# Optimization experiments

Measured on AMD Instinct MI355X. Metric: run time of the kernel, lower is better.

Reference implementation:

```python
import jax, jax.numpy as jnp
import numpy as np

N_FFT = 4096
HOP = 1024
HALF = N_FFT // 2  # 2048; also number of freq bins is HALF+1 = 2049


def _make_kernels():
    # Periodic hann window, matching torch.hann_window(N) default (periodic=True)
    n = np.arange(N_FFT, dtype=np.float32)
    window = 0.5 * (1.0 - np.cos(2.0 * np.pi * n / N_FFT))
    freqs = np.arange(HALF + 1, dtype=np.float32)[:, None]  # [K,1]
    omega = 2.0 * np.pi * freqs * n[None, :] / N_FFT        # [K, n_fft]
    scale = np.float32(1.0 / np.sqrt(N_FFT))                # normalized=True
    cos_k = (np.cos(omega) * window[None, :] * scale).astype(np.float32)
    sin_k = (-np.sin(omega) * window[None, :] * scale).astype(np.float32)
    return jnp.asarray(cos_k), jnp.asarray(sin_k)


def setup_inputs() -> dict:
    key = jax.random.key(0)
    x = jax.random.normal(key, (32, 1, 441000), dtype=jnp.float32)
    cos_kernel, sin_kernel = _make_kernels()  # each [2049, 4096]
    return {"x": x, "cos_kernel": cos_kernel, "sin_kernel": sin_kernel}


def reference(x, cos_kernel, sin_kernel):
    # center=True: reflect-pad half_n_fft on each side of the time axis
    xp = jnp.pad(x, ((0, 0), (0, 0), (HALF, HALF)), mode='reflect')  # [B,1,L]
    L = xp.shape[-1]
    num_frames = (L - N_FFT) // HOP + 1
    # Frame extraction (equivalent to stride-HOP conv1d with width-N_FFT kernels)
    idx = HOP * jnp.arange(num_frames)[:, None] + jnp.arange(N_FFT)[None, :]  # [F, n_fft]
    frames = xp[:, 0, :][:, idx]  # [B, F, n_fft]
    real = jnp.einsum('bfn,kn->bkf', frames, cos_kernel)  # [B, 2049, F]
    imag = jnp.einsum('bfn,kn->bkf', frames, sin_kernel)  # [B, 2049, F]
    return jnp.stack((real, imag), axis=-1)  # [B, 2049, F, 2]
```

## Files before the change

kernel.cpp:

```cpp
#include <hip/hip_runtime.h>
#include <math.h>

#define NFFT  4096
#define MHALF 2048
#define HOPSZ 1024
#define LX    441000
#define NB    32
#define NF    431
#define NK    2049
#define NFPB  8
#define FBLK  54
#define NWG3  (NB * FBLK)
#define CH3   (NWG3 / 8)

#define SW(A) ((A) ^ (((A) >> 4) & 0xF))
#define SOFTSYNC() asm volatile("" ::: "memory")

typedef __fp16 half2v __attribute__((ext_vector_type(2)));

__device__ __forceinline__ float2 cadd(float2 a, float2 b){ return make_float2(a.x+b.x, a.y+b.y); }
__device__ __forceinline__ float2 csub(float2 a, float2 b){ return make_float2(a.x-b.x, a.y-b.y); }
__device__ __forceinline__ float2 cmul(float2 a, float2 b){
  return make_float2(fmaf(a.x, b.x, -(a.y*b.y)), fmaf(a.x, b.y, a.y*b.x));
}
#define STH(ptr, idx, v) (ptr)[idx] = __builtin_amdgcn_cvt_pkrtz((v).x, (v).y)
__device__ __forceinline__ float2 ldh(const half2v* __restrict__ X, int idx) {
  half2v h = X[idx];
  return make_float2((float)h.x, (float)h.y);
}

constexpr float W32C[22] = {
  1.0f, 0.98078528040323f, 0.92387953251129f, 0.83146961230255f, 0.70710678118655f,
  0.55557023301960f, 0.38268343236509f, 0.19509032201613f, 0.0f, -0.19509032201613f,
  -0.38268343236509f, -0.55557023301960f, -0.70710678118655f, -0.83146961230255f,
  -0.92387953251129f, -0.98078528040323f, -1.0f, -0.98078528040323f,
  -0.92387953251129f, -0.83146961230255f, -0.70710678118655f, -0.55557023301960f };
constexpr float W32S[22] = {
  0.0f, 0.19509032201613f, 0.38268343236509f, 0.55557023301960f, 0.70710678118655f,
  0.83146961230255f, 0.92387953251129f, 0.98078528040323f, 1.0f, 0.98078528040323f,
  0.92387953251129f, 0.83146961230255f, 0.70710678118655f, 0.55557023301960f,
  0.38268343236509f, 0.19509032201613f, 0.0f, -0.19509032201613f,
  -0.38268343236509f, -0.55557023301960f, -0.70710678118655f, -0.83146961230255f };

template<int N> __device__ __forceinline__ float2 w32m(float2 z) {
  if constexpr (N == 0) { return z; }
  else if constexpr (N == 8) { return make_float2(z.y, -z.x); }
  else {
    constexpr float c = W32C[N];
    constexpr float s = W32S[N];
    return make_float2(fmaf(z.x, c, z.y * s), fmaf(z.y, c, -(z.x * s)));
  }
}

__global__ void stft_init(float* __restrict__ ws) {
  int i = blockIdx.x * blockDim.x + threadIdx.x;
  const double PI = 3.14159265358979323846;
  if (i < 4096) {
    double w = 0.5 * (1.0 - cos(2.0 * PI * (double)i / 4096.0)) * (1.0 / 64.0);
    ws[i] = (float)w;
  }
  if (i < 1024) {
    double a = -2.0 * PI * (double)i / 2048.0;
    ws[4096 + 2 * i]     = (float)cos(a);
    ws[4096 + 2 * i + 1] = (float)sin(a);
  }
  if (i < 2049) {
    double a = -2.0 * PI * (double)i / 4096.0;
    ws[6144 + 2 * i]     = (float)cos(a);
    ws[6144 + 2 * i + 1] = (float)sin(a);
  }
}

__device__ __forceinline__ void dft8(const float2* a, float2* B) {
  float2 t0 = cadd(a[0], a[4]), t1 = csub(a[0], a[4]);
  float2 t2 = cadd(a[2], a[6]), t3 = csub(a[2], a[6]);
  float2 t4 = cadd(a[1], a[5]), t5 = csub(a[1], a[5]);
  float2 t6 = cadd(a[3], a[7]), t7 = csub(a[3], a[7]);
  const float K = 0.70710678118654752f;
  float2 wt5  = make_float2(K * (t5.x + t5.y), K * (t5.y - t5.x));
  float2 w3t7 = make_float2(K * (t7.y - t7.x), -K * (t7.x + t7.y));
  float2 wt7  = make_float2(K * (t7.x + t7.y), K * (t7.y - t7.x));
  float2 w3t5 = make_float2(K * (t5.y - t5.x), -K * (t5.x + t5.y));
  float2 e0 = cadd(t0, t2), e1 = csub(t0, t2);
  float2 f0 = cadd(t4, t6), f1 = csub(t4, t6);
  B[0] = cadd(e0, f0);
  B[4] = csub(e0, f0);
  B[2] = make_float2(e1.x + f1.y, e1.y - f1.x);
  B[6] = make_float2(e1.x - f1.y, e1.y + f1.x);
  float2 g0 = make_float2(t1.x + t3.y, t1.y - t3.x);
  float2 g1 = make_float2(t1.x - t3.y, t1.y + t3.x);
  float2 h0 = cadd(wt5, w3t7);
  float2 h1 = cadd(wt7, w3t5);
  B[1] = cadd(g0, h0);
  B[5] = csub(g0, h0);
  B[3] = cadd(g1, h1);
  B[7] = csub(g1, h1);
}

template<int S>
__device__ __forceinline__ void bf8(half2v* __restrict__ X, int sxor,
                                    const float2* __restrict__ twg,
                                    int j, const float2* a) {
  const int q = j & (S - 1);
  const int t = j - q;
  float2 B[8];
  dft8(a, B);
  float2 w1 = twg[t];
  float2 w2 = cmul(w1, w1);
  float2 w3 = cmul(w2, w1);
  float2 w4 = cmul(w2, w2);
  float2 w5 = cmul(w3, w2);
  float2 w6 = cmul(w3, w3);
  float2 w7 = cmul(w4, w3);
  const int o = q + 8 * t;
  STH(X, SW(o) ^ sxor, B[0]);
  { float2 v = cmul(w1, B[1]); STH(X, SW(o + S)     ^ sxor, v); }
  { float2 v = cmul(w2, B[2]); STH(X, SW(o + 2 * S) ^ sxor, v); }
  { float2 v = cmul(w3, B[3]); STH(X, SW(o + 3 * S) ^ sxor, v); }
  { float2 v = cmul(w4, B[4]); STH(X, SW(o + 4 * S) ^ sxor, v); }
  { float2 v = cmul(w5, B[5]); STH(X, SW(o + 5 * S) ^ sxor, v); }
  { float2 v = cmul(w6, B[6]); STH(X, SW(o + 6 * S) ^ sxor, v); }
  { float2 v = cmul(w7, B[7]); STH(X, SW(o + 7 * S) ^ sxor, v); }
}

__device__ __forceinline__ void loadwin(float2 (*a)[8], const float* __restrict__ xb,
                                        int f, int l,
                                        const float2* __restrict__ winv,
                                        const float* __restrict__ win) {
  const int base = f * HOPSZ - MHALF;
  if (base >= 0 && base + NFFT <= LX) {
    const float2* xv = (const float2*)(xb + base);
#pragma unroll
    for (int r = 0; r < 4; ++r) {
      const int j = l + (r << 6);
#pragma unroll
      for (int m = 0; m < 8; ++m) {
        const int idx = j + (m << 8);
        float2 v = xv[idx];
        float2 w = winv[idx];
        a[r][m] = make_float2(v.x * w.x, v.y * w.y);
      }
    }
  } else {
#pragma unroll
    for (int r = 0; r < 4; ++r) {
      const int j = l + (r << 6);
#pragma unroll
      for (int m = 0; m < 8; ++m) {
        const int idx = j + (m << 8);
        int s0 = base + 2 * idx;
        int s1 = s0 + 1;
        s0 = (s0 < 0) ? -s0 : ((s0 >= LX) ? (2 * LX - 2 - s0) : s0);
        s1 = (s1 < 0) ? -s1 : ((s1 >= LX) ? (2 * LX - 2 - s1) : s1);
        a[r][m] = make_float2(xb[s0] * win[2 * idx], xb[s1] * win[2 * idx + 1]);
      }
    }
  }
}

#define VBLK(dd, slp, sx, V) do {                                     \
    float2 tt[8], BB[8];                                              \
    tt[0] = dd[8*(V)+0];                                              \
    tt[1] = w32m<1*(V)>(dd[8*(V)+1]);                                 \
    tt[2] = w32m<2*(V)>(dd[8*(V)+2]);                                 \
    tt[3] = w32m<3*(V)>(dd[8*(V)+3]);                                 \
    tt[4] = w32m<4*(V)>(dd[8*(V)+4]);                                 \
    tt[5] = w32m<5*(V)>(dd[8*(V)+5]);                                 \
    tt[6] = w32m<6*(V)>(dd[8*(V)+6]);                                 \
    tt[7] = w32m<7*(V)>(dd[8*(V)+7]);                                 \
    dft8(tt, BB);                                                     \
    STH(slp, SW(l + (((V) +  0) << 6)) ^ sx, BB[0]);                  \
    STH(slp, SW(l + (((V) +  4) << 6)) ^ sx, BB[1]);                  \
    STH(slp, SW(l + (((V) +  8) << 6)) ^ sx, BB[2]);                  \
    STH(slp, SW(l + (((V) + 12) << 6)) ^ sx, BB[3]);                  \
    STH(slp, SW(l + (((V) + 16) << 6)) ^ sx, BB[4]);                  \
    STH(slp, SW(l + (((V) + 20) << 6)) ^ sx, BB[5]);                  \
    STH(slp, SW(l + (((V) + 24) << 6)) ^ sx, BB[6]);                  \
    STH(slp, SW(l + (((V) + 28) << 6)) ^ sx, BB[7]);                  \
  } while (0)

#define DFT4PASS(dd) do {                                             \
    _Pragma("unroll")                                                 \
    for (int m1 = 0; m1 < 8; ++m1) {                                  \
      float2 p0 = dd[m1], p1 = dd[m1 + 8], p2 = dd[m1 + 16], p3 = dd[m1 + 24]; \
      float2 e0 = cadd(p0, p2), e1 = csub(p0, p2);                    \
      float2 o0 = cadd(p1, p3), o1 = csub(p1, p3);                    \
      dd[m1]      = cadd(e0, o0);                                     \
      dd[m1 + 8]  = make_float2(e1.x + o1.y, e1.y - o1.x);            \
      dd[m1 + 16] = csub(e0, o0);                                     \
      dd[m1 + 24] = make_float2(e1.x - o1.y, e1.y + o1.x);            \
    }                                                                 \
  } while (0)

__global__ __launch_bounds__(256, 2) void stft_fft(const float* __restrict__ x,
                                                   const float* __restrict__ ws,
                                                   float* __restrict__ out) {
  __shared__ half2v fbuf[NFPB * 2048];

  const int tid = threadIdx.x;
  const int wid = (blockIdx.x & 7) * CH3 + (blockIdx.x >> 3);
  const int b  = wid / FBLK;
  const int fb = wid - b * FBLK;
  const int f0 = fb * NFPB;
  const int wv = tid >> 6;
  const int l  = tid & 63;
  const int fA = f0 + 2 * wv;
  const int fB = fA + 1;
  const bool hasB = (fB < NF);

  const float*  win  = ws;
  const float2* winv = (const float2*)ws;
  const float2* twg  = (const float2*)(ws + 4096);
  const float2* tw4  = (const float2*)(ws + 6144);
  const float* xb = x + (size_t)b * LX;

  half2v* __restrict__ slA = &fbuf[(2 * wv) * 2048];
  half2v* __restrict__ slB = &fbuf[(2 * wv + 1) * 2048];
  const int sxA = (2 * wv) << 2;
  const int sxB = (2 * wv + 1) << 2;

  {
    float2 aA[4][8], aB[4][8];
    loadwin(aA, xb, fA, l, winv, win);
    if (hasB) loadwin(aB, xb, fB, l, winv, win);
#pragma unroll
    for (int r = 0; r < 4; ++r) {
      bf8<1>(slA, sxA, twg, l + (r << 6), aA[r]);
      if (hasB) bf8<1>(slB, sxB, twg, l + (r << 6), aB[r]);
    }
    SOFTSYNC();

#pragma unroll
    for (int r = 0; r < 4; ++r) {
      const int j = l + (r << 6);
#pragma unroll
      for (int m = 0; m < 8; ++m) {
        aA[r][m] = ldh(slA, SW(j + (m << 8)) ^ sxA);
        if (hasB) aB[r][m] = ldh(slB, SW(j + (m << 8)) ^ sxB);
      }
    }
    SOFTSYNC();
#pragma unroll
    for (int r = 0; r < 4; ++r) {
      bf8<8>(slA, sxA, twg, l + (r << 6), aA[r]);
      if (hasB) bf8<8>(slB, sxB, twg, l + (r << 6), aB[r]);
    }
    SOFTSYNC();
  }

  {
    float2 dA[32], dB[32];
#pragma unroll
    for (int m = 0; m < 32; ++m) {
      dA[m] = ldh(slA, SW(l + (m << 6)) ^ sxA);
      if (hasB) dB[m] = ldh(slB, SW(l + (m << 6)) ^ sxB);
    }
    SOFTSYNC();
    DFT4PASS(dA);
    VBLK(dA, slA, sxA, 0); VBLK(dA, slA, sxA, 1);
    VBLK(dA, slA, sxA, 2); VBLK(dA, slA, sxA, 3);
    if (hasB) {
      DFT4PASS(dB);
      VBLK(dB, slB, sxB, 0); VBLK(dB, slB, sxB, 1);
      VBLK(dB, slB, sxB, 2); VBLK(dB, slB, sxB, 3);
    }
  }
  __syncthreads();

  float2* __restrict__ op = (float2*)out;
  const size_t obB = (size_t)b * NK * NF;
  const int s  = tid & 7;
  const int kk = tid >> 3;
  const int fS = f0 + s;
  const bool act = (fS < NF);
  const half2v* __restrict__ sl2 = &fbuf[s * 2048];
  const int sx2 = s << 2;
#pragma unroll 4
  for (int it = 0; it < 32; ++it) {
    const int k  = kk + (it << 5);
    const int km = (2048 - k) & 2047;
    float2 zk = ldh(sl2, SW(k)  ^ sx2);
    float2 zm = ldh(sl2, SW(km) ^ sx2);
    float xex = 0.5f * (zk.x + zm.x);
    float xey = 0.5f * (zk.y - zm.y);
    float xox = 0.5f * (zk.y + zm.y);
    float xoy = 0.5f * (zm.x - zk.x);
    float2 w = tw4[k];
    float tx = w.x * xox - w.y * xoy;
    float ty = w.x * xoy + w.y * xox;
    if (act) {
      op[obB + (size_t)k * NF + fS]          = make_float2(xex + tx,  xey + ty);
      op[obB + (size_t)(2048 - k) * NF + fS] = make_float2(xex - tx, -xey + ty);
    }
  }
  if (tid < 8 && (f0 + tid) < NF) {
    const half2v* slt = &fbuf[tid * 2048];
    float2 zq = ldh(slt, SW(1024) ^ (tid << 2));
    op[obB + (size_t)1024 * NF + (f0 + tid)] = make_float2(zq.x, -zq.y);
  }
}

extern "C" void kernel_launch(void* const* d_in, const int* in_sizes, int n_in,
                              void* d_out, int out_size, void* d_ws, size_t ws_size,
                              hipStream_t stream) {
  const float* x = (const float*)d_in[0];
  float* ws = (float*)d_ws;
  float* out = (float*)d_out;
  stft_init<<<16, 256, 0, stream>>>(ws);
  stft_fft<<<NWG3, 256, 0, stream>>>(x, ws, out);
}
```

Before: 130.1 us.

## Replace LDS-based FFT stages with register and wavefront-shuffle butterflies

The 2048-point complex FFT per frame is restructured so each wavefront owns one frame. The first 32-point stages run in registers, and the remaining radix-2 stages use cross-lane __shfl_xor exchanges of fp16-packed values instead of LDS round trips. Block size grows to 512 threads with one frame per wave, and the LDS swizzle and output layout are changed to match. This removes intermediate shared-memory passes but adds many shuffles and fp16 rounding at every exchange stage, plus register pressure under launch_bounds(512,4).

```diff
diff --git a/kernel.cpp b/kernel.cpp
--- a/kernel.cpp
+++ b/kernel.cpp
@@ -13,19 +13,22 @@
 #define NWG3  (NB * FBLK)
 #define CH3   (NWG3 / 8)
 
-#define SW(A) ((A) ^ (((A) >> 4) & 0xF))
-#define SOFTSYNC() asm volatile("" ::: "memory")
-
-typedef __fp16 half2v __attribute__((ext_vector_type(2)));
+#define SW2(A) ((A) ^ (((A) >> 5) & 31))
+#define PHYS(K) (((((K) & 3)) << 3) | ((K) >> 2))
+
+typedef __fp16 h2v __attribute__((ext_vector_type(2)));
 
 __device__ __forceinline__ float2 cadd(float2 a, float2 b){ return make_float2(a.x+b.x, a.y+b.y); }
 __device__ __forceinline__ float2 csub(float2 a, float2 b){ return make_float2(a.x-b.x, a.y-b.y); }
 __device__ __forceinline__ float2 cmul(float2 a, float2 b){
   return make_float2(fmaf(a.x, b.x, -(a.y*b.y)), fmaf(a.x, b.y, a.y*b.x));
 }
-#define STH(ptr, idx, v) (ptr)[idx] = __builtin_amdgcn_cvt_pkrtz((v).x, (v).y)
-__device__ __forceinline__ float2 ldh(const half2v* __restrict__ X, int idx) {
-  half2v h = X[idx];
+__device__ __forceinline__ unsigned pk2(float2 v) {
+  h2v h = __builtin_amdgcn_cvt_pkrtz(v.x, v.y);
+  return __builtin_bit_cast(unsigned, h);
+}
+__device__ __forceinline__ float2 unpk2(unsigned u) {
+  h2v h = __builtin_bit_cast(h2v, u);
   return make_float2((float)h.x, (float)h.y);
 }
 
@@ -97,88 +100,6 @@
   B[7] = csub(g1, h1);
 }
 
-template<int S>
-__device__ __forceinline__ void bf8(half2v* __restrict__ X, int sxor,
-                                    const float2* __restrict__ twg,
-                                    int j, const float2* a) {
-  const int q = j & (S - 1);
-  const int t = j - q;
-  float2 B[8];
-  dft8(a, B);
-  float2 w1 = twg[t];
-  float2 w2 = cmul(w1, w1);
-  float2 w3 = cmul(w2, w1);
-  float2 w4 = cmul(w2, w2);
-  float2 w5 = cmul(w3, w2);
-  float2 w6 = cmul(w3, w3);
-  float2 w7 = cmul(w4, w3);
-  const int o = q + 8 * t;
-  STH(X, SW(o) ^ sxor, B[0]);
-  { float2 v = cmul(w1, B[1]); STH(X, SW(o + S)     ^ sxor, v); }
-  { float2 v = cmul(w2, B[2]); STH(X, SW(o + 2 * S) ^ sxor, v); }
-  { float2 v = cmul(w3, B[3]); STH(X, SW(o + 3 * S) ^ sxor, v); }
-  { float2 v = cmul(w4, B[4]); STH(X, SW(o + 4 * S) ^ sxor, v); }
-  { float2 v = cmul(w5, B[5]); STH(X, SW(o + 5 * S) ^ sxor, v); }
-  { float2 v = cmul(w6, B[6]); STH(X, SW(o + 6 * S) ^ sxor, v); }
-  { float2 v = cmul(w7, B[7]); STH(X, SW(o + 7 * S) ^ sxor, v); }
-}
-
-__device__ __forceinline__ void loadwin(float2 (*a)[8], const float* __restrict__ xb,
-                                        int f, int l,
-                                        const float2* __restrict__ winv,
-                                        const float* __restrict__ win) {
-  const int base = f * HOPSZ - MHALF;
-  if (base >= 0 && base + NFFT <= LX) {
-    const float2* xv = (const float2*)(xb + base);
-#pragma unroll
-    for (int r = 0; r < 4; ++r) {
-      const int j = l + (r << 6);
-#pragma unroll
-      for (int m = 0; m < 8; ++m) {
-        const int idx = j + (m << 8);
-        float2 v = xv[idx];
-        float2 w = winv[idx];
-        a[r][m] = make_float2(v.x * w.x, v.y * w.y);
-      }
-    }
-  } else {
-#pragma unroll
-    for (int r = 0; r < 4; ++r) {
-      const int j = l + (r << 6);
-#pragma unroll
-      for (int m = 0; m < 8; ++m) {
-        const int idx = j + (m << 8);
-        int s0 = base + 2 * idx;
-        int s1 = s0 + 1;
-        s0 = (s0 < 0) ? -s0 : ((s0 >= LX) ? (2 * LX - 2 - s0) : s0);
-        s1 = (s1 < 0) ? -s1 : ((s1 >= LX) ? (2 * LX - 2 - s1) : s1);
-        a[r][m] = make_float2(xb[s0] * win[2 * idx], xb[s1] * win[2 * idx + 1]);
-      }
-    }
-  }
-}
-
-#define VBLK(dd, slp, sx, V) do {                                     \
-    float2 tt[8], BB[8];                                              \
-    tt[0] = dd[8*(V)+0];                                              \
-    tt[1] = w32m<1*(V)>(dd[8*(V)+1]);                                 \
-    tt[2] = w32m<2*(V)>(dd[8*(V)+2]);                                 \
-    tt[3] = w32m<3*(V)>(dd[8*(V)+3]);                                 \
-    tt[4] = w32m<4*(V)>(dd[8*(V)+4]);                                 \
-    tt[5] = w32m<5*(V)>(dd[8*(V)+5]);                                 \
-    tt[6] = w32m<6*(V)>(dd[8*(V)+6]);                                 \
-    tt[7] = w32m<7*(V)>(dd[8*(V)+7]);                                 \
-    dft8(tt, BB);                                                     \
-    STH(slp, SW(l + (((V) +  0) << 6)) ^ sx, BB[0]);                  \
-    STH(slp, SW(l + (((V) +  4) << 6)) ^ sx, BB[1]);                  \
-    STH(slp, SW(l + (((V) +  8) << 6)) ^ sx, BB[2]);                  \
-    STH(slp, SW(l + (((V) + 12) << 6)) ^ sx, BB[3]);                  \
-    STH(slp, SW(l + (((V) + 16) << 6)) ^ sx, BB[4]);                  \
-    STH(slp, SW(l + (((V) + 20) << 6)) ^ sx, BB[5]);                  \
-    STH(slp, SW(l + (((V) + 24) << 6)) ^ sx, BB[6]);                  \
-    STH(slp, SW(l + (((V) + 28) << 6)) ^ sx, BB[7]);                  \
-  } while (0)
-
 #define DFT4PASS(dd) do {                                             \
     _Pragma("unroll")                                                 \
     for (int m1 = 0; m1 < 8; ++m1) {                                  \
@@ -192,10 +113,39 @@
     }                                                                 \
   } while (0)
 
-__global__ __launch_bounds__(256, 2) void stft_fft(const float* __restrict__ x,
+#define VBLKR(dd, V) do {                                             \
+    float2 tt[8], BB[8];                                              \
+    tt[0] = dd[8*(V)+0];                                              \
+    tt[1] = w32m<1*(V)>(dd[8*(V)+1]);                                 \
+    tt[2] = w32m<2*(V)>(dd[8*(V)+2]);                                 \
+    tt[3] = w32m<3*(V)>(dd[8*(V)+3]);                                 \
+    tt[4] = w32m<4*(V)>(dd[8*(V)+4]);                                 \
+    tt[5] = w32m<5*(V)>(dd[8*(V)+5]);                                 \
+    tt[6] = w32m<6*(V)>(dd[8*(V)+6]);                                 \
+    tt[7] = w32m<7*(V)>(dd[8*(V)+7]);                                 \
+    dft8(tt, BB);                                                     \
+    dd[8*(V)+0] = BB[0]; dd[8*(V)+1] = BB[1];                         \
+    dd[8*(V)+2] = BB[2]; dd[8*(V)+3] = BB[3];                         \
+    dd[8*(V)+4] = BB[4]; dd[8*(V)+5] = BB[5];                         \
+    dd[8*(V)+6] = BB[6]; dd[8*(V)+7] = BB[7];                         \
+  } while (0)
+
+#define XSTAGE(dd, M, WS, HI) do {                                    \
+    _Pragma("unroll")                                                 \
+    for (int p = 0; p < 32; ++p) {                                    \
+      float2 vv = dd[p];                                              \
+      float2 vp = unpk2((unsigned)__shfl_xor((int)pk2(vv), (M)));     \
+      float2 sm = cadd(vv, vp);                                       \
+      float2 df = csub(vp, vv);                                       \
+      float2 dw = cmul(df, (WS));                                     \
+      dd[p] = (HI) ? dw : sm;                                         \
+    }                                                                 \
+  } while (0)
+
+__global__ __launch_bounds__(512, 4) void stft_fft(const float* __restrict__ x,
                                                    const float* __restrict__ ws,
                                                    float* __restrict__ out) {
-  __shared__ half2v fbuf[NFPB * 2048];
+  __shared__ unsigned zbuf[NFPB * 2048];
 
   const int tid = threadIdx.x;
   const int wid = (blockIdx.x & 7) * CH3 + (blockIdx.x >> 3);
@@ -204,9 +154,7 @@
   const int f0 = fb * NFPB;
   const int wv = tid >> 6;
   const int l  = tid & 63;
-  const int fA = f0 + 2 * wv;
-  const int fB = fA + 1;
-  const bool hasB = (fB < NF);
+  const int f  = f0 + wv;
 
   const float*  win  = ws;
   const float2* winv = (const float2*)ws;
@@ -214,55 +162,84 @@
   const float2* tw4  = (const float2*)(ws + 6144);
   const float* xb = x + (size_t)b * LX;
 
-  half2v* __restrict__ slA = &fbuf[(2 * wv) * 2048];
-  half2v* __restrict__ slB = &fbuf[(2 * wv + 1) * 2048];
-  const int sxA = (2 * wv) << 2;
-  const int sxB = (2 * wv + 1) << 2;
-
-  {
-    float2 aA[4][8], aB[4][8];
-    loadwin(aA, xb, fA, l, winv, win);
-    if (hasB) loadwin(aB, xb, fB, l, winv, win);
-#pragma unroll
-    for (int r = 0; r < 4; ++r) {
-      bf8<1>(slA, sxA, twg, l + (r << 6), aA[r]);
-      if (hasB) bf8<1>(slB, sxB, twg, l + (r << 6), aB[r]);
-    }
-    SOFTSYNC();
-
-#pragma unroll
-    for (int r = 0; r < 4; ++r) {
-      const int j = l + (r << 6);
-#pragma unroll
-      for (int m = 0; m < 8; ++m) {
-        aA[r][m] = ldh(slA, SW(j + (m << 8)) ^ sxA);
-        if (hasB) aB[r][m] = ldh(slB, SW(j + (m << 8)) ^ sxB);
-      }
-    }
-    SOFTSYNC();
-#pragma unroll
-    for (int r = 0; r < 4; ++r) {
-      bf8<8>(slA, sxA, twg, l + (r << 6), aA[r]);
-      if (hasB) bf8<8>(slB, sxB, twg, l + (r << 6), aB[r]);
-    }
-    SOFTSYNC();
-  }
-
-  {
-    float2 dA[32], dB[32];
-#pragma unroll
-    for (int m = 0; m < 32; ++m) {
-      dA[m] = ldh(slA, SW(l + (m << 6)) ^ sxA);
-      if (hasB) dB[m] = ldh(slB, SW(l + (m << 6)) ^ sxB);
-    }
-    SOFTSYNC();
-    DFT4PASS(dA);
-    VBLK(dA, slA, sxA, 0); VBLK(dA, slA, sxA, 1);
-    VBLK(dA, slA, sxA, 2); VBLK(dA, slA, sxA, 3);
-    if (hasB) {
-      DFT4PASS(dB);
-      VBLK(dB, slB, sxB, 0); VBLK(dB, slB, sxB, 1);
-      VBLK(dB, slB, sxB, 2); VBLK(dB, slB, sxB, 3);
+  if (f < NF) {
+    float2 d[32];
+    const int base = f * HOPSZ - MHALF;
+    if (base >= 0 && base + NFFT <= LX) {
+      const float2* xv = (const float2*)(xb + base);
+#pragma unroll
+      for (int m = 0; m < 32; ++m) {
+        const int idx = l + (m << 6);
+        float2 v = xv[idx];
+        float2 w = winv[idx];
+        d[m] = make_float2(v.x * w.x, v.y * w.y);
+      }
+    } else {
+#pragma unroll
+      for (int m = 0; m < 32; ++m) {
+        const int idx = l + (m << 6);
+        int s0 = base + 2 * idx;
+        int s1 = s0 + 1;
+        s0 = (s0 < 0) ? -s0 : ((s0 >= LX) ? (2 * LX - 2 - s0) : s0);
+        s1 = (s1 < 0) ? -s1 : ((s1 >= LX) ? (2 * LX - 2 - s1) : s1);
+        d[m] = make_float2(xb[s0] * win[2 * idx], xb[s1] * win[2 * idx + 1]);
+      }
+    }
+
+    DFT4PASS(d);
+    VBLKR(d, 0); VBLKR(d, 1); VBLKR(d, 2); VBLKR(d, 3);
+
+    {
+      const float2 wl = twg[l];
+      float2 wp = wl;
+      d[PHYS(1)] = cmul(d[PHYS(1)], wp);
+#pragma unroll
+      for (int q = 2; q < 32; ++q) {
+        wp = cmul(wp, wl);
+        d[PHYS(q)] = cmul(d[PHYS(q)], wp);
+      }
+    }
+
+    {
+      const float2 s32 = twg[(l & 31) << 5];
+      const float2 s16 = twg[(l & 15) << 6];
+      const float2 s8v = twg[(l & 7)  << 7];
+      const float2 s4v = twg[(l & 3)  << 8];
+      XSTAGE(d, 32, s32, (l & 32));
+      XSTAGE(d, 16, s16, (l & 16));
+      XSTAGE(d,  8, s8v, (l & 8));
+      XSTAGE(d,  4, s4v, (l & 4));
+      {
+        const bool odd = (l & 1), hi = (l & 2);
+#pragma unroll
+        for (int p = 0; p < 32; ++p) {
+          float2 vv = d[p];
+          float2 vp = unpk2((unsigned)__shfl_xor((int)pk2(vv), 2));
+          float2 sm = cadd(vv, vp);
+          float2 df = csub(vp, vv);
+          float2 dw = odd ? make_float2(df.y, -df.x) : df;
+          d[p] = hi ? dw : sm;
+        }
+      }
+      {
+        const bool hi = (l & 1);
+#pragma unroll
+        for (int p = 0; p < 32; ++p) {
+          float2 vv = d[p];
+          float2 vp = unpk2((unsigned)__shfl_xor((int)pk2(vv), 1));
+          d[p] = hi ? csub(vp, vv) : cadd(vv, vp);
+        }
+      }
+    }
+
+    {
+      const int B = ((l&1)<<5)|((l&2)<<3)|((l&4)<<1)|((l&8)>>1)|((l&16)>>3)|((l&32)>>5);
+      unsigned* __restrict__ sl = &zbuf[wv * 2048];
+      const int sx = wv << 2;
+#pragma unroll
+      for (int q = 0; q < 32; ++q) {
+        sl[SW2(q + (B << 5)) ^ sx] = pk2(d[PHYS(q)]);
+      }
     }
   }
   __syncthreads();
@@ -273,14 +250,14 @@
   const int kk = tid >> 3;
   const int fS = f0 + s;
   const bool act = (fS < NF);
-  const half2v* __restrict__ sl2 = &fbuf[s * 2048];
+  const unsigned* __restrict__ sl2 = &zbuf[s * 2048];
   const int sx2 = s << 2;
 #pragma unroll 4
-  for (int it = 0; it < 32; ++it) {
-    const int k  = kk + (it << 5);
+  for (int it = 0; it < 16; ++it) {
+    const int k  = kk + (it << 6);
     const int km = (2048 - k) & 2047;
-    float2 zk = ldh(sl2, SW(k)  ^ sx2);
-    float2 zm = ldh(sl2, SW(km) ^ sx2);
+    float2 zk = unpk2(sl2[SW2(k)  ^ sx2]);
+    float2 zm = unpk2(sl2[SW2(km) ^ sx2]);
     float xex = 0.5f * (zk.x + zm.x);
     float xey = 0.5f * (zk.y - zm.y);
     float xox = 0.5f * (zk.y + zm.y);
@@ -294,8 +271,7 @@
     }
   }
   if (tid < 8 && (f0 + tid) < NF) {
-    const half2v* slt = &fbuf[tid * 2048];
-    float2 zq = ldh(slt, SW(1024) ^ (tid << 2));
+    float2 zq = unpk2(zbuf[tid * 2048 + (SW2(1024) ^ (tid << 2))]);
     op[obB + (size_t)1024 * NF + (f0 + tid)] = make_float2(zq.x, -zq.y);
   }
 }
@@ -307,5 +283,5 @@
   float* ws = (float*)d_ws;
   float* out = (float*)d_out;
   stft_init<<<16, 256, 0, stream>>>(ws);
-  stft_fft<<<NWG3, 256, 0, stream>>>(x, ws, out);
-}
+  stft_fft<<<NWG3, 512, 0, stream>>>(x, ws, out);
+}
```

After: 141.8 us. 1.09x slower.
